# Performance work log

Measured on AMD Instinct MI355X. Metric: run time of the kernel, lower is better.

The kernel has to match this reference:

```python
import jax, jax.numpy as jnp
import numpy as np

NUM_CAPSULE = 10
DIM_CAPSULE = 16
ROUTINGS = 3
EPS = 1e-7  # K.epsilon()


def squash(x, axis=-1):
    # bojone squash: x / sqrt(s2 + eps) * s2 / (1 + s2)
    s2 = jnp.sum(jnp.square(x), axis=axis, keepdims=True)
    return x * s2 / ((1.0 + s2) * jnp.sqrt(s2 + EPS))


def setup_inputs() -> dict:
    key = jax.random.key(0)
    k1, k2 = jax.random.split(key)
    B, N, D_in = 64, 2048, 128  # batch, input_num_capsule, input_dim_capsule
    u_vecs = jax.random.normal(k1, (B, N, D_in), dtype=jnp.float32)
    fan_out = NUM_CAPSULE * DIM_CAPSULE
    limit = float(np.sqrt(6.0 / (D_in + fan_out)))  # glorot_uniform
    W = jax.random.uniform(k2, (D_in, fan_out), dtype=jnp.float32,
                           minval=-limit, maxval=limit)
    return {"u_vecs": u_vecs, "W": W}


def reference(u_vecs, W):
    B, N, _ = u_vecs.shape
    # share_weights=True: conv1d with kernel size 1 == matmul over feature dim
    u_hat = (u_vecs @ W).reshape(B, N, NUM_CAPSULE, DIM_CAPSULE)
    u_hat = jnp.transpose(u_hat, (0, 2, 1, 3))  # (B, J, N, D)
    b = jnp.zeros((B, NUM_CAPSULE, N), dtype=u_vecs.dtype)
    o = jnp.zeros((B, NUM_CAPSULE, DIM_CAPSULE), dtype=u_vecs.dtype)
    for i in range(ROUTINGS):
        c = jax.nn.softmax(b, axis=1)           # softmax over output capsules
        o = jnp.einsum('bjn,bjnd->bjd', c, u_hat)
        if i < ROUTINGS - 1:
            b = jnp.einsum('bjd,bjnd->bjn', o, u_hat)  # agreement update
    return squash(o)
```

## Files before the change

kernel.cpp:

```cpp
#include <hip/hip_runtime.h>
#include <math.h>


#define BATCH 64
#define NN    2048
#define KD    128
#define JCAP  10
#define DCAP  16
#define JDIM  160
#define EPSQ  1e-7f
#define NT    64
#define TROW  32

#define WS_GP 0
#define WS_V  (BATCH * NT * JCAP * KD)

__device__ __forceinline__ void gload16(const float* g, void* l) {
  __builtin_amdgcn_global_load_lds(
      (const __attribute__((address_space(1))) void*)g,
      (__attribute__((address_space(3))) void*)l, 16, 0, 0);
}

__global__ __launch_bounds__(256) void f_iter0(const float* __restrict__ u,
                                               float* __restrict__ Sp) {
  const int b = blockIdx.y, tile = blockIdx.x, t = threadIdx.x;
  __shared__ __align__(16) float4 red[256];
  const int c = t & 31, rg = t >> 5;
  const float* p = u + (((size_t)(b * NN + tile * TROW + rg * 4)) << 7) + (c << 2);
  float4 a = make_float4(0.f, 0.f, 0.f, 0.f);
#pragma unroll
  for (int r = 0; r < 4; ++r) {
    const float4 w4 = *(const float4*)(p + ((size_t)r << 7));
    a.x += w4.x; a.y += w4.y; a.z += w4.z; a.w += w4.w;
  }
  red[t] = a;
  __syncthreads();
  if (t < 32) {
    float4 s4 = red[t];
#pragma unroll
    for (int g = 1; g < 8; ++g) {
      const float4 w4 = red[g * 32 + t];
      s4.x += w4.x; s4.y += w4.y; s4.z += w4.z; s4.w += w4.w;
    }
    *(float4*)&Sp[(size_t)(b * NT + tile) * KD + t * 4] = s4;
  }
}

__global__ __launch_bounds__(128) void f_fold(const float* __restrict__ In,
                                              const float* __restrict__ W,
                                              float* __restrict__ Out, int pass) {
  const int j = blockIdx.x, b = blockIdx.y, t = threadIdx.x;
  __shared__ float g_s[KD];
  __shared__ float o_s[DCAP];
  if (pass == 0) {
    const float* p = In + (size_t)b * NT * KD + t;
    float s = 0.f;
#pragma unroll 8
    for (int tl = 0; tl < NT; ++tl) s += p[(size_t)tl * KD];
    g_s[t] = s * 0.1f;
  } else {
    const float* p = In + ((size_t)(b * NT) * JCAP + j) * KD + t;
    float s = 0.f;
#pragma unroll 8
    for (int tl = 0; tl < NT; ++tl) s += p[(size_t)tl * JCAP * KD];
    g_s[t] = s;
  }
  __syncthreads();
  if (t < DCAP) {
    float a = 0.f;
#pragma unroll 8
    for (int k = 0; k < KD; ++k) a += g_s[k] * W[k * JDIM + j * DCAP + t];
    o_s[t] = a;
  }
  __syncthreads();
  if (pass < 2) {
    const float* wp = W + t * JDIM + j * DCAP;
    float a = 0.f;
#pragma unroll
    for (int d = 0; d < DCAP; ++d) a += wp[d] * o_s[d];
    Out[((size_t)(b * JCAP) + j) * KD + t] = a;
  } else if (t < DCAP) {
    float s2 = 0.f;
#pragma unroll
    for (int d = 0; d < DCAP; ++d) s2 += o_s[d] * o_s[d];
    const float sc = s2 / ((1.f + s2) * sqrtf(s2 + EPSQ));
    Out[(size_t)(b * JCAP + j) * DCAP + t] = o_s[t] * sc;
  }
}

__global__ __launch_bounds__(256) void f_route(const float* __restrict__ u,
                                               const float* __restrict__ V,
                                               float* __restrict__ Gp) {
  const int b = blockIdx.y, tile = blockIdx.x, t = threadIdx.x;
  const int w = t >> 6, l = t & 63;
  __shared__ __align__(16) float4 u4[TROW * 32];
  __shared__ __align__(16) float4 Vs4[JCAP * 32];
  __shared__ __align__(16) float Cs[JCAP * TROW];

  {
    const float* ub = u + (((size_t)(b * NN + tile * TROW)) << 7);
#pragma unroll
    for (int p = 0; p < 4; ++p) {
      const int df = (w << 8) + (p << 6);
      const int s = df + l;
      const int r = s >> 5, pos = s & 31;
      const int L = pos ^ (r & 7);
      gload16(ub + (((size_t)r) << 7) + (L << 2), &u4[df]);
    }
    const float* vb = V + (((size_t)(b * JCAP)) << 7);
#pragma unroll
    for (int q = 0; q < 5; ++q)
      gload16(vb + ((q * 64 + l) << 2), &Vs4[q * 64]);
  }
  asm volatile("s_waitcnt vmcnt(0)" ::: "memory");
  __builtin_amdgcn_sched_barrier(0);

  {
    const int rx = l >> 3, kq = l & 7;
    const int r = (w << 3) + rx;
    float4 ur[4];
#pragma unroll
    for (int c = 0; c < 4; ++c) ur[c] = u4[(r << 5) + ((c * 8 + kq) ^ rx)];
    float acc[JCAP];
#pragma unroll
    for (int j = 0; j < JCAP; ++j) acc[j] = 0.f;
#pragma unroll
    for (int c = 0; c < 4; ++c) {
#pragma unroll
      for (int j = 0; j < JCAP; ++j) {
        const float4 vv = Vs4[j * 32 + c * 8 + kq];
        acc[j] += ur[c].x * vv.x + ur[c].y * vv.y + ur[c].z * vv.z + ur[c].w * vv.w;
      }
    }
#pragma unroll
    for (int j = 0; j < JCAP; ++j) {
      acc[j] += __shfl_xor(acc[j], 1, 64);
      acc[j] += __shfl_xor(acc[j], 2, 64);
      acc[j] += __shfl_xor(acc[j], 4, 64);
    }
    if (kq == 0) {
      float m = acc[0];
#pragma unroll
      for (int j = 1; j < JCAP; ++j) m = fmaxf(m, acc[j]);
      float ss = 0.f;
#pragma unroll
      for (int j = 0; j < JCAP; ++j) { acc[j] = __expf(acc[j] - m); ss += acc[j]; }
      const float inv = 1.f / ss;
#pragma unroll
      for (int j = 0; j < JCAP; ++j) Cs[j * TROW + r] = acc[j] * inv;
    }
  }
  __syncthreads();

  {
    const int j0 = (w < 2) ? 3 * w : 2 * w + 2;
    const int jn = (w < 2) ? 3 : 2;
    const int chalf = l >> 1, cin = (l & 1) << 1;
    float g0[3], g1[3];
#pragma unroll
    for (int jj = 0; jj < 3; ++jj) { g0[jj] = 0.f; g1[jj] = 0.f; }
#pragma unroll
    for (int o = 0; o < 4; ++o) {
      float ua[8], uc[8];
#pragma unroll
      for (int ri = 0; ri < 8; ++ri) {
        const int r = o * 8 + ri;
        const float2 uu2 =
            *(const float2*)((const float*)&u4[(r << 5) + (chalf ^ ri)] + cin);
        ua[ri] = uu2.x; uc[ri] = uu2.y;
      }
#pragma unroll
      for (int jj = 0; jj < 3; ++jj) {
        if (jj < jn) {
          const float4 cA = *(const float4*)&Cs[(j0 + jj) * TROW + o * 8];
          const float4 cB = *(const float4*)&Cs[(j0 + jj) * TROW + o * 8 + 4];
          g0[jj] += cA.x * ua[0] + cA.y * ua[1] + cA.z * ua[2] + cA.w * ua[3]
                  + cB.x * ua[4] + cB.y * ua[5] + cB.z * ua[6] + cB.w * ua[7];
          g1[jj] += cA.x * uc[0] + cA.y * uc[1] + cA.z * uc[2] + cA.w * uc[3]
                  + cB.x * uc[4] + cB.y * uc[5] + cB.z * uc[6] + cB.w * uc[7];
        }
      }
    }
    float* gb = Gp + ((size_t)(b * NT + tile)) * JCAP * KD;
#pragma unroll
    for (int jj = 0; jj < 3; ++jj)
      if (jj < jn)
        *(float2*)&gb[(j0 + jj) * KD + 2 * l] = make_float2(g0[jj], g1[jj]);
  }
}

extern "C" void kernel_launch(void* const* d_in, const int* in_sizes, int n_in,
                              void* d_out, int out_size, void* d_ws, size_t ws_size,
                              hipStream_t stream) {
  const float* u = (const float*)d_in[0];
  const float* W = (const float*)d_in[1];
  float* out = (float*)d_out;
  float* ws  = (float*)d_ws;

  float* Gp = ws + WS_GP;
  float* V  = ws + WS_V;
  f_iter0 <<<dim3(NT, BATCH), 256, 0, stream>>>(u, Gp);
  f_fold  <<<dim3(JCAP, BATCH), 128, 0, stream>>>(Gp, W, V, 0);
  f_route <<<dim3(NT, BATCH), 256, 0, stream>>>(u, V, Gp);
  f_fold  <<<dim3(JCAP, BATCH), 128, 0, stream>>>(Gp, W, V, 1);
  f_route <<<dim3(NT, BATCH), 256, 0, stream>>>(u, V, Gp);
  f_fold  <<<dim3(JCAP, BATCH), 128, 0, stream>>>(Gp, W, out, 2);
}
```

Baseline: 172.4 us.

## Read V straight from global and restructure route accumulation with float4 row splits

f_route stops staging V in LDS and reads each V float4 straight from global (cache-resident) memory inside the agreement loop. The weighted-sum phase moves from float2 column pairs over 8 rows to float4 columns over 4 rows per half-wave, combined with a cross-half shuffle reduction and float4 stores. A launch-bounds occupancy hint of 8 blocks is added. This cuts LDS footprint and LDS read instructions, at the cost of more global/L1 loads and extra shuffles.

```diff
diff --git a/kernel.cpp b/kernel.cpp
--- a/kernel.cpp
+++ b/kernel.cpp
@@ -88,13 +88,12 @@
   }
 }
 
-__global__ __launch_bounds__(256) void f_route(const float* __restrict__ u,
-                                               const float* __restrict__ V,
-                                               float* __restrict__ Gp) {
+__global__ __launch_bounds__(256, 8) void f_route(const float* __restrict__ u,
+                                                  const float* __restrict__ V,
+                                                  float* __restrict__ Gp) {
   const int b = blockIdx.y, tile = blockIdx.x, t = threadIdx.x;
   const int w = t >> 6, l = t & 63;
   __shared__ __align__(16) float4 u4[TROW * 32];
-  __shared__ __align__(16) float4 Vs4[JCAP * 32];
   __shared__ __align__(16) float Cs[JCAP * TROW];
 
   {
@@ -107,10 +106,6 @@
       const int L = pos ^ (r & 7);
       gload16(ub + (((size_t)r) << 7) + (L << 2), &u4[df]);
     }
-    const float* vb = V + (((size_t)(b * JCAP)) << 7);
-#pragma unroll
-    for (int q = 0; q < 5; ++q)
-      gload16(vb + ((q * 64 + l) << 2), &Vs4[q * 64]);
   }
   asm volatile("s_waitcnt vmcnt(0)" ::: "memory");
   __builtin_amdgcn_sched_barrier(0);
@@ -121,14 +116,16 @@
     float4 ur[4];
 #pragma unroll
     for (int c = 0; c < 4; ++c) ur[c] = u4[(r << 5) + ((c * 8 + kq) ^ rx)];
+    const float* vb = V + (((size_t)(b * JCAP)) << 7);
     float acc[JCAP];
 #pragma unroll
     for (int j = 0; j < JCAP; ++j) acc[j] = 0.f;
 #pragma unroll
     for (int c = 0; c < 4; ++c) {
+      const int vo = (c * 8 + kq) << 2;
 #pragma unroll
       for (int j = 0; j < JCAP; ++j) {
-        const float4 vv = Vs4[j * 32 + c * 8 + kq];
+        const float4 vv = *(const float4*)(vb + (j << 7) + vo);
         acc[j] += ur[c].x * vv.x + ur[c].y * vv.y + ur[c].z * vv.z + ur[c].w * vv.w;
       }
     }
@@ -155,37 +152,46 @@
   {
     const int j0 = (w < 2) ? 3 * w : 2 * w + 2;
     const int jn = (w < 2) ? 3 : 2;
-    const int chalf = l >> 1, cin = (l & 1) << 1;
-    float g0[3], g1[3];
-#pragma unroll
-    for (int jj = 0; jj < 3; ++jj) { g0[jj] = 0.f; g1[jj] = 0.f; }
+    const int c4 = l & 31, h = l >> 5;
+    const int c4h = c4 ^ (h << 2);
+    float4 g[3];
+#pragma unroll
+    for (int jj = 0; jj < 3; ++jj) g[jj] = make_float4(0.f, 0.f, 0.f, 0.f);
 #pragma unroll
     for (int o = 0; o < 4; ++o) {
-      float ua[8], uc[8];
-#pragma unroll
-      for (int ri = 0; ri < 8; ++ri) {
-        const int r = o * 8 + ri;
-        const float2 uu2 =
-            *(const float2*)((const float*)&u4[(r << 5) + (chalf ^ ri)] + cin);
-        ua[ri] = uu2.x; uc[ri] = uu2.y;
+      float4 uo[4];
+#pragma unroll
+      for (int i = 0; i < 4; ++i) {
+        const int r = (o << 3) + (h << 2) + i;
+        uo[i] = u4[(r << 5) + (c4h ^ i)];
       }
 #pragma unroll
       for (int jj = 0; jj < 3; ++jj) {
         if (jj < jn) {
-          const float4 cA = *(const float4*)&Cs[(j0 + jj) * TROW + o * 8];
-          const float4 cB = *(const float4*)&Cs[(j0 + jj) * TROW + o * 8 + 4];
-          g0[jj] += cA.x * ua[0] + cA.y * ua[1] + cA.z * ua[2] + cA.w * ua[3]
-                  + cB.x * ua[4] + cB.y * ua[5] + cB.z * ua[6] + cB.w * ua[7];
-          g1[jj] += cA.x * uc[0] + cA.y * uc[1] + cA.z * uc[2] + cA.w * uc[3]
-                  + cB.x * uc[4] + cB.y * uc[5] + cB.z * uc[6] + cB.w * uc[7];
+          const float4 cs = *(const float4*)&Cs[(j0 + jj) * TROW + (o << 3) + (h << 2)];
+          g[jj].x += cs.x * uo[0].x + cs.y * uo[1].x + cs.z * uo[2].x + cs.w * uo[3].x;
+          g[jj].y += cs.x * uo[0].y + cs.y * uo[1].y + cs.z * uo[2].y + cs.w * uo[3].y;
+          g[jj].z += cs.x * uo[0].z + cs.y * uo[1].z + cs.z * uo[2].z + cs.w * uo[3].z;
+          g[jj].w += cs.x * uo[0].w + cs.y * uo[1].w + cs.z * uo[2].w + cs.w * uo[3].w;
         }
       }
     }
-    float* gb = Gp + ((size_t)(b * NT + tile)) * JCAP * KD;
-#pragma unroll
-    for (int jj = 0; jj < 3; ++jj)
-      if (jj < jn)
-        *(float2*)&gb[(j0 + jj) * KD + 2 * l] = make_float2(g0[jj], g1[jj]);
+#pragma unroll
+    for (int jj = 0; jj < 3; ++jj) {
+      if (jj < jn) {
+        g[jj].x += __shfl_xor(g[jj].x, 32, 64);
+        g[jj].y += __shfl_xor(g[jj].y, 32, 64);
+        g[jj].z += __shfl_xor(g[jj].z, 32, 64);
+        g[jj].w += __shfl_xor(g[jj].w, 32, 64);
+      }
+    }
+    if (h == 0) {
+      float* gb = Gp + ((size_t)(b * NT + tile)) * JCAP * KD;
+#pragma unroll
+      for (int jj = 0; jj < 3; ++jj)
+        if (jj < jn)
+          *(float4*)&gb[(j0 + jj) * KD + (c4 << 2)] = g[jj];
+    }
   }
 }
 
```

After: 361.8 us. 110% more time.
